# Kernel tuning notes

Measured on AMD Instinct MI355X. Metric: run time of the kernel, lower is better.

The kernel has to match this reference:

```python
import jax, jax.numpy as jnp
import numpy as np
from jax import lax

DIM = 512
HEADS = 8
HEAD_DIM = DIM // HEADS
FS = 56            # features_size -> H = W = 56
SR = 2             # sr_ratio
N = FS * FS        # query tokens = 3136
KN = (FS // SR) ** 2  # kv tokens = 784
B = 4
SCALE = HEAD_DIM ** -0.5
LN_EPS = 1e-5


def _relative_indices(fs):
    # matches generate_relative_distance: [[x, y] for x in range(fs) for y in range(fs)]
    coords = np.stack(np.meshgrid(np.arange(fs), np.arange(fs), indexing='ij'), -1).reshape(-1, 2)
    dist = coords[None, :, :] - coords[:, None, :] + (fs - 1)   # (N, N, 2), values in [0, 2fs-2]
    return jnp.asarray(dist, dtype=jnp.int32)


def setup_inputs() -> dict:
    key = jax.random.key(0)
    ks = jax.random.split(key, 8)
    s = 0.02
    return {
        'x':    jax.random.normal(ks[0], (B, DIM, FS, FS), jnp.float32),
        'Wq':   jax.random.normal(ks[1], (DIM, DIM), jnp.float32) * s,
        'Wkv':  jax.random.normal(ks[2], (DIM, 2 * DIM), jnp.float32) * s,
        'Wsr':  jax.random.normal(ks[3], (DIM, DIM, SR, SR), jnp.float32) * s,  # OIHW
        'b_sr': jnp.zeros((DIM,), jnp.float32),
        'gamma': jnp.ones((DIM,), jnp.float32),
        'beta':  jnp.zeros((DIM,), jnp.float32),
        'Wp':   jax.random.normal(ks[4], (DIM, DIM), jnp.float32) * s,
        'bp':   jnp.zeros((DIM,), jnp.float32),
        'pos':  jax.random.normal(ks[5], (2 * FS - 1, 2 * FS - 1), jnp.float32) * 0.2,
        'rel_idx': _relative_indices(FS),
    }


def reference(x, Wq, Wkv, Wsr, b_sr, gamma, beta, Wp, bp, pos, rel_idx):
    b, c, h, w = x.shape
    n = h * w
    xq = x.reshape(b, c, n).transpose(0, 2, 1)                      # B N C
    q = (xq @ Wq).reshape(b, n, HEADS, HEAD_DIM).transpose(0, 2, 1, 3)  # B h N d

    # spatial reduction of k/v: Conv2d(k=SR, s=SR) + LayerNorm
    xr = lax.conv_general_dilated(x, Wsr, (SR, SR), 'VALID',
                                  dimension_numbers=('NCHW', 'OIHW', 'NCHW'))
    xr = xr + b_sr[None, :, None, None]
    kn = xr.shape[2] * xr.shape[3]
    xkv = xr.reshape(b, c, kn).transpose(0, 2, 1)                   # B KN C
    mu = xkv.mean(-1, keepdims=True)
    var = ((xkv - mu) ** 2).mean(-1, keepdims=True)
    xkv = (xkv - mu) * lax.rsqrt(var + LN_EPS) * gamma + beta

    # kv projection; rearrange 'B N (dim h l) -> l B h N dim'
    kv = (xkv @ Wkv).reshape(b, kn, HEAD_DIM, HEADS, 2)
    k = kv[..., 0].transpose(0, 3, 1, 2)                            # B h KN d
    v = kv[..., 1].transpose(0, 3, 1, 2)                            # B h KN d

    attn = jnp.einsum('bhnd,bhmd->bhnm', q, k) * SCALE              # B h N KN
    bias = pos[rel_idx[:, :kn, 0], rel_idx[:, :kn, 1]]              # N KN gathered bias
    attn = jax.nn.softmax(attn + bias, axis=-1)

    out = jnp.einsum('bhnm,bhmd->bhnd', attn, v)                    # B h N d
    out = out.transpose(0, 2, 1, 3).reshape(b, n, c)                # B N C
    out = out @ Wp + bp
    return out.transpose(0, 2, 1).reshape(b, c, h, w)
```

## Files before the change

kernel.cpp:

```cpp
#include <hip/hip_runtime.h>
#include <hip/hip_bf16.h>
#include <cstdint>

constexpr int BATCH = 4;
constexpr int CDIM  = 512;
constexpr int NHEAD = 8;
constexpr int HD    = 64;
constexpr int FSP   = 56;
constexpr int NTOK  = FSP * FSP;
constexpr int KH    = 28;
constexpr int KNTOK = KH * KH;
constexpr float SCALE_ATT = 0.125f;
constexpr int BIAS_LD = 832;

typedef _Float16 f16;
typedef __attribute__((ext_vector_type(8))) _Float16 half8;
typedef __attribute__((ext_vector_type(4))) float  floatx4;

__device__ __forceinline__ void tr64(const float* __restrict__ in,
                                     f16* __restrict__ out, int R, int C,
                                     int r0, int c0, float (*sm)[65], int tid) {
  const int rr = tid >> 2, cs = (tid & 3) * 16;
  const float* src = in + (size_t)(r0 + rr) * C + c0 + cs;
#pragma unroll
  for (int j = 0; j < 16; j += 4) *(float4*)&sm[rr][cs + j] = *(const float4*)&src[j];
  __syncthreads();
  f16* dh = out + (size_t)(c0 + rr) * R + r0 + cs;
#pragma unroll
  for (int j = 0; j < 16; ++j) dh[j] = (f16)sm[cs + j][rr];
}

__global__ __launch_bounds__(256) void k_prep(const float* __restrict__ x,
                                              const float* __restrict__ Wq,
                                              const float* __restrict__ Wkv,
                                              const float* __restrict__ Wp,
                                              const float* __restrict__ Wsr,
                                              const int* __restrict__ rel,
                                              const float* __restrict__ pos,
                                              f16* __restrict__ xT,
                                              f16* __restrict__ WqT,
                                              f16* __restrict__ WkvT,
                                              f16* __restrict__ WpT,
                                              f16* __restrict__ WsrP,
                                              float* __restrict__ biasT) {
  __shared__ float sm[64][65];
  const int tid = threadIdx.x;
  int bid = blockIdx.x;
  if (bid < 1568) {
    const int b = bid / 392, r = bid % 392;
    tr64(x + (size_t)b * CDIM * NTOK, xT + (size_t)b * NTOK * CDIM,
         CDIM, NTOK, (r % 8) * 64, (r / 8) * 64, sm, tid);
    return;
  }
  bid -= 1568;
  if (bid < 64)  { tr64(Wq,  WqT,  512, 512,  (bid % 8) * 64, (bid / 8) * 64, sm, tid); return; }
  bid -= 64;
  if (bid < 128) { tr64(Wkv, WkvT, 512, 1024, (bid % 8) * 64, (bid / 8) * 64, sm, tid); return; }
  bid -= 128;
  if (bid < 64)  { tr64(Wp,  WpT,  512, 512,  (bid % 8) * 64, (bid / 8) * 64, sm, tid); return; }
  bid -= 64;
  if (bid < 512) {
    const float* src = Wsr + (size_t)bid * 2048;
    f16* dh = WsrP + (size_t)bid * 2048;
    for (int kp = tid; kp < 2048; kp += 256) {
      const int dd = kp >> 9, c = kp & 511;
      dh[kp] = (f16)src[c * 4 + dd];
    }
    return;
  }
  bid -= 512;
  {
    const int n = bid;
    for (int i = tid; i < BIAS_LD; i += 256) {
      const int jc = i >> 6, w = i & 63, txx = w >> 2, tt = w & 3;
      const int m = jc * 64 + tt * 16 + txx;
      float v = -30000.f;
      if (m < KNTOK) {
        const size_t o = ((size_t)n * NTOK + m) * 2;
        v = pos[rel[o] * 111 + rel[o + 1]];
      }
      biasT[(size_t)n * BIAS_LD + i] = v;
    }
  }
}

#define GSTR 40
struct GemmSmem { f16 A[64][GSTR]; f16 B[128][GSTR]; };

__device__ __forceinline__ void gemm_loop64(GemmSmem* sm,
    const f16* __restrict__ aP, const f16* __restrict__ bP, bool doA,
    int sr, int ss, int wm, int wn, int quad, int tx, floatx4 acc[2][4]) {
  half8 ra0 = {0, 0, 0, 0, 0, 0, 0, 0}, ra1 = ra0;
  if (doA) { ra0 = *(const half8*)&aP[0]; ra1 = *(const half8*)&aP[8]; }
  half8 rb0 = *(const half8*)&bP[0], rb1 = *(const half8*)&bP[8];
  for (int it = 0; it < 16; ++it) {
    if (doA) { *(half8*)&sm->A[sr][ss] = ra0; *(half8*)&sm->A[sr][ss + 8] = ra1; }
    *(half8*)&sm->B[sr][ss] = rb0; *(half8*)&sm->B[sr][ss + 8] = rb1;
    __syncthreads();
    if (it + 1 < 16) {
      const f16* an = aP + (it + 1) * 32;
      const f16* bn = bP + (it + 1) * 32;
      if (doA) { ra0 = *(const half8*)&an[0]; ra1 = *(const half8*)&an[8]; }
      rb0 = *(const half8*)&bn[0]; rb1 = *(const half8*)&bn[8];
    }
    half8 ah[2];
#pragma unroll
    for (int i = 0; i < 2; ++i)
      ah[i] = *(const half8*)&sm->A[wm * 32 + i * 16 + tx][quad * 8];
#pragma unroll
    for (int j = 0; j < 4; ++j) {
      const half8 bh = *(const half8*)&sm->B[wn * 64 + j * 16 + tx][quad * 8];
#pragma unroll
      for (int i = 0; i < 2; ++i)
        acc[i][j] = __builtin_amdgcn_mfma_f32_16x16x32_f16(ah[i], bh, acc[i][j], 0, 0, 0);
    }
    __syncthreads();
  }
}

#define GEMM_PRE64()                                                      \
  const int tid = threadIdx.x, lane = tid & 63, wv = tid >> 6;            \
  const int wm = wv & 1, wn = wv >> 1, quad = lane >> 4, tx = lane & 15;  \
  const int sr = tid >> 1, ss = (tid & 1) * 16;                           \
  const bool doA = tid < 128;                                             \
  floatx4 acc[2][4];                                                      \
  _Pragma("unroll") for (int i = 0; i < 2; ++i)                           \
  _Pragma("unroll") for (int j = 0; j < 4; ++j)                           \
      acc[i][j] = (floatx4){0.f, 0.f, 0.f, 0.f};

__global__ __launch_bounds__(256) void k_gemmA(const f16* __restrict__ xT,
                                               const f16* __restrict__ WqT,
                                               f16* __restrict__ Qh,
                                               const f16* __restrict__ WsrP,
                                               float* __restrict__ XRp) {
  __shared__ GemmSmem sm;
  GEMM_PRE64();
  int bid = blockIdx.x;
  if (bid < 784) {
    const int b = bid / 196, r = bid % 196;
    const int m0 = (r >> 2) * 64, n0 = (r & 3) * 128;
    const f16* aP = xT + (size_t)b * NTOK * CDIM + (size_t)(m0 + sr) * CDIM + ss;
    const f16* bP = WqT + (size_t)(n0 + sr) * CDIM + ss;
    gemm_loop64(&sm, aP, bP, doA, sr, ss, wm, wn, quad, tx, acc);
    f16* qhB = Qh + (size_t)b * NTOK * CDIM;
#pragma unroll
    for (int i = 0; i < 2; ++i)
#pragma unroll
      for (int rg = 0; rg < 4; ++rg) {
        const int m = m0 + wm * 32 + i * 16 + quad * 4 + rg;
#pragma unroll
        for (int j = 0; j < 4; ++j)
          qhB[(size_t)m * CDIM + n0 + wn * 64 + j * 16 + tx] = (f16)acc[i][j][rg];
      }
  } else {
    bid -= 784;
    const int bkc = bid / 52, r = bid % 52;
    const int b = bkc >> 2, kc = bkc & 3;
    const int m0 = (r >> 2) * 64, n0 = (r & 3) * 128;
    int am = m0 + sr; if (am >= KNTOK) am = 0;
    const int ii = am / KH, jj = am % KH;
    const int sp = 112 * ii + 2 * jj + (kc >> 1) * FSP + (kc & 1);
    const f16* aP = xT + (size_t)b * NTOK * CDIM + (size_t)sp * CDIM + ss;
    const f16* bP = WsrP + (size_t)(n0 + sr) * 2048 + kc * 512 + ss;
    gemm_loop64(&sm, aP, bP, doA, sr, ss, wm, wn, quad, tx, acc);
    float* dst = XRp + (size_t)(kc * BATCH + b) * KNTOK * CDIM;
#pragma unroll
    for (int i = 0; i < 2; ++i)
#pragma unroll
      for (int rg = 0; rg < 4; ++rg) {
        const int m = m0 + wm * 32 + i * 16 + quad * 4 + rg;
        if (m >= KNTOK) continue;
#pragma unroll
        for (int j = 0; j < 4; ++j)
          dst[(size_t)m * CDIM + n0 + wn * 64 + j * 16 + tx] = acc[i][j][rg];
      }
  }
}

__global__ __launch_bounds__(256) void k_ln(const float* __restrict__ XRp,
                                            const float* __restrict__ b_sr,
                                            const float* __restrict__ gamma,
                                            const float* __restrict__ beta,
                                            f16* __restrict__ oh) {
  const int row = blockIdx.x;
  const size_t slab = (size_t)BATCH * KNTOK * CDIM;
  const float* p = XRp + (size_t)row * CDIM;
  const int tid = threadIdx.x;
  const float v0 = p[tid] + p[tid + slab] + p[tid + 2 * slab] + p[tid + 3 * slab]
                 + b_sr[tid];
  const float v1 = p[tid + 256] + p[tid + 256 + slab] + p[tid + 256 + 2 * slab]
                 + p[tid + 256 + 3 * slab] + b_sr[tid + 256];
  float s = v0 + v1;
  float s2 = v0 * v0 + v1 * v1;
#pragma unroll
  for (int mask = 32; mask >= 1; mask >>= 1) {
    s  += __shfl_xor(s, mask, 64);
    s2 += __shfl_xor(s2, mask, 64);
  }
  __shared__ float ws[4], ws2[4];
  const int wid = tid >> 6;
  if ((tid & 63) == 0) { ws[wid] = s; ws2[wid] = s2; }
  __syncthreads();
  const float ts  = ws[0] + ws[1] + ws[2] + ws[3];
  const float ts2 = ws2[0] + ws2[1] + ws2[2] + ws2[3];
  const float mu  = ts * (1.f / CDIM);
  const float var = ts2 * (1.f / CDIM) - mu * mu;
  const float rs  = rsqrtf(var + 1e-5f);
  const size_t base = (size_t)row * CDIM;
  oh[base + tid]       = (f16)((v0 - mu) * rs * gamma[tid] + beta[tid]);
  oh[base + tid + 256] = (f16)((v1 - mu) * rs * gamma[tid + 256] + beta[tid + 256]);
}

__global__ __launch_bounds__(256) void k_kvproj(const f16* __restrict__ XRh,
                                                const f16* __restrict__ WkvT,
                                                f16* __restrict__ Kh,
                                                f16* __restrict__ Vt) {
  __shared__ GemmSmem sm;
  GEMM_PRE64();
  const int bid = blockIdx.x;
  const int b = bid / 104, r = bid % 104;
  const int m0 = (r >> 3) * 64, n0 = (r & 7) * 128;
  int arow = m0 + sr; if (arow >= KNTOK) arow = KNTOK - 1;
  const f16* aP = XRh + (size_t)b * KNTOK * CDIM + (size_t)arow * CDIM + ss;
  const f16* bP = WkvT + (size_t)(n0 + sr) * CDIM + ss;
  gemm_loop64(&sm, aP, bP, doA, sr, ss, wm, wn, quad, tx, acc);
#pragma unroll
  for (int i = 0; i < 2; ++i)
#pragma unroll
    for (int rg = 0; rg < 4; ++rg) {
      const int m = m0 + wm * 32 + i * 16 + quad * 4 + rg;
      if (m >= KNTOK) continue;
#pragma unroll
      for (int j = 0; j < 4; ++j) {
        const int o2 = n0 + wn * 64 + j * 16 + tx;
        const int d = o2 >> 4, hh = (o2 >> 1) & 7;
        const float v = acc[i][j][rg];
        if (o2 & 1)
          Vt[((size_t)(b * NHEAD + hh) * HD + d) * KNTOK + m] = (f16)v;
        else
          Kh[((size_t)(b * NHEAD + hh) * KNTOK + m) * HD + d] = (f16)v;
      }
    }
}

#define LSTR 72
__global__ __launch_bounds__(256) void k_attn(const f16* __restrict__ Qh,
                                              const f16* __restrict__ Kh,
                                              const f16* __restrict__ Vt,
                                              const float* __restrict__ biasT,
                                              f16* __restrict__ Oh) {
  __shared__ f16 Qhs[64][LSTR], Khs[64][LSTR], Vts[64][LSTR];
  __shared__ f16 Ps[4][16][LSTR];
  const int b = blockIdx.x >> 3, h = blockIdx.x & 7;
  const int n0 = blockIdx.y * 64;
  const int tid = threadIdx.x, lane = tid & 63, wv = tid >> 6;
  const int quad = lane >> 4, tx = lane & 15;
  const int rr = tid >> 2, sg = (tid & 3) * 16;

  const f16* qhB = Qh + ((size_t)b * NTOK + n0) * CDIM + h * HD;
  const f16* khB = Kh + (size_t)(b * NHEAD + h) * KNTOK * HD;
  const f16* vtB = Vt + (size_t)(b * NHEAD + h) * HD * KNTOK;

  {
    const size_t qoff = (size_t)rr * CDIM + sg;
    *(half8*)&Qhs[rr][sg]     = *(const half8*)&qhB[qoff];
    *(half8*)&Qhs[rr][sg + 8] = *(const half8*)&qhB[qoff + 8];
    const size_t koff = (size_t)rr * HD + sg;
    *(half8*)&Khs[rr][sg]     = *(const half8*)&khB[koff];
    *(half8*)&Khs[rr][sg + 8] = *(const half8*)&khB[koff + 8];
    const size_t voff = (size_t)rr * KNTOK + sg;
    *(half8*)&Vts[rr][sg]     = *(const half8*)&vtB[voff];
    *(half8*)&Vts[rr][sg + 8] = *(const half8*)&vtB[voff + 8];
  }

  size_t bbase_r[4];
#pragma unroll
  for (int r = 0; r < 4; ++r)
    bbase_r[r] = (size_t)(n0 + wv * 16 + quad * 4 + r) * BIAS_LD + tx * 4;

  floatx4 acc_o[4];
#pragma unroll
  for (int t = 0; t < 4; ++t) acc_o[t] = (floatx4){0.f, 0.f, 0.f, 0.f};
  float l_part[4] = {0.f, 0.f, 0.f, 0.f};
  __syncthreads();

  half8 nk0, nk1, nv0, nv1;
  for (int jc = 0; jc < 13; ++jc) {
    if (jc < 12) {
      const int mbn = (jc + 1) * 64;
      const int km = min(mbn + rr, KNTOK - 1);
      const size_t koff = (size_t)km * HD + sg;
      nk0 = *(const half8*)&khB[koff];
      nk1 = *(const half8*)&khB[koff + 8];
      const int vc = min(mbn + sg, KNTOK - 16);
      const size_t voff = (size_t)rr * KNTOK + vc;
      nv0 = *(const half8*)&vtB[voff];
      nv1 = *(const half8*)&vtB[voff + 8];
    }

    floatx4 sc[4];
#pragma unroll
    for (int t = 0; t < 4; ++t) sc[t] = (floatx4){0.f, 0.f, 0.f, 0.f};
#pragma unroll
    for (int ks = 0; ks < 2; ++ks) {
      const int kk = ks * 32 + quad * 8;
      const half8 aqh = *(const half8*)&Qhs[wv * 16 + tx][kk];
#pragma unroll
      for (int t = 0; t < 4; ++t) {
        const half8 bkh = *(const half8*)&Khs[t * 16 + tx][kk];
        sc[t] = __builtin_amdgcn_mfma_f32_16x16x32_f16(aqh, bkh, sc[t], 0, 0, 0);
      }
    }

#pragma unroll
    for (int r = 0; r < 4; ++r) {
      const float4 bb = *(const float4*)&biasT[bbase_r[r] + jc * 64];
      const float p0 = __expf(fmaf(sc[0][r], SCALE_ATT, bb.x));
      const float p1 = __expf(fmaf(sc[1][r], SCALE_ATT, bb.y));
      const float p2 = __expf(fmaf(sc[2][r], SCALE_ATT, bb.z));
      const float p3 = __expf(fmaf(sc[3][r], SCALE_ATT, bb.w));
      l_part[r] += (p0 + p1) + (p2 + p3);
      const int prow = quad * 4 + r;
      Ps[wv][prow][0 * 16 + tx] = (f16)p0;
      Ps[wv][prow][1 * 16 + tx] = (f16)p1;
      Ps[wv][prow][2 * 16 + tx] = (f16)p2;
      Ps[wv][prow][3 * 16 + tx] = (f16)p3;
    }

#pragma unroll
    for (int ks = 0; ks < 2; ++ks) {
      const int kk = ks * 32 + quad * 8;
      const half8 ap = *(const half8*)&Ps[wv][tx][kk];
#pragma unroll
      for (int t = 0; t < 4; ++t) {
        const half8 bv = *(const half8*)&Vts[t * 16 + tx][kk];
        acc_o[t] = __builtin_amdgcn_mfma_f32_16x16x32_f16(ap, bv, acc_o[t], 0, 0, 0);
      }
    }
    __syncthreads();
    if (jc < 12) {
      *(half8*)&Khs[rr][sg]     = nk0;
      *(half8*)&Khs[rr][sg + 8] = nk1;
      *(half8*)&Vts[rr][sg]     = nv0;
      *(half8*)&Vts[rr][sg + 8] = nv1;
    }
    __syncthreads();
  }

#pragma unroll
  for (int r = 0; r < 4; ++r) {
    float l = l_part[r];
#pragma unroll
    for (int msk = 1; msk < 16; msk <<= 1) l += __shfl_xor(l, msk, 64);
    const float inv = 1.f / l;
    const int grow = n0 + wv * 16 + quad * 4 + r;
    const size_t base = ((size_t)b * NTOK + grow) * CDIM + h * HD;
#pragma unroll
    for (int t = 0; t < 4; ++t)
      Oh[base + t * 16 + tx] = (f16)(acc_o[t][r] * inv);
  }
}

__global__ __launch_bounds__(256) void k_outproj(const f16* __restrict__ Og,
                                                 const f16* __restrict__ WpT,
                                                 const float* __restrict__ bp,
                                                 float* __restrict__ out) {
  __shared__ GemmSmem sm;
  GEMM_PRE64();
  const int bid = blockIdx.x;
  const int b = bid / 196, r = bid % 196;
  const int m0 = (r >> 2) * 64, n0 = (r & 3) * 128;
  const f16* aP = Og + (size_t)b * NTOK * CDIM + (size_t)(m0 + sr) * CDIM + ss;
  const f16* bP = WpT + (size_t)(n0 + sr) * CDIM + ss;
  gemm_loop64(&sm, aP, bP, doA, sr, ss, wm, wn, quad, tx, acc);
#pragma unroll
  for (int j = 0; j < 4; ++j) {
    const int co = n0 + wn * 64 + j * 16 + tx;
    const float bpv = bp[co];
    float* obase = out + ((size_t)b * CDIM + co) * NTOK;
#pragma unroll
    for (int i = 0; i < 2; ++i) {
      const int mb4 = m0 + wm * 32 + i * 16 + quad * 4;
      floatx4 v = acc[i][j] + bpv;
      *(floatx4*)&obase[mb4] = v;
    }
  }
}

extern "C" void kernel_launch(void* const* d_in, const int* in_sizes, int n_in,
                              void* d_out, int out_size, void* d_ws, size_t ws_size,
                              hipStream_t stream) {
  const float* x     = (const float*)d_in[0];
  const float* Wq    = (const float*)d_in[1];
  const float* Wkv   = (const float*)d_in[2];
  const float* Wsr   = (const float*)d_in[3];
  const float* b_sr  = (const float*)d_in[4];
  const float* gamma = (const float*)d_in[5];
  const float* beta  = (const float*)d_in[6];
  const float* Wp    = (const float*)d_in[7];
  const float* bp    = (const float*)d_in[8];
  const float* pos   = (const float*)d_in[9];
  const int*   rel   = (const int*)d_in[10];
  float* out = (float*)d_out;

  char* p = (char*)d_ws;
  auto alloc = [&](size_t bytes) -> void* {
    void* r = (void*)p;
    p += (bytes + 255) & ~(size_t)255;
    return r;
  };
  const size_t SZ_BNC = (size_t)BATCH * NTOK * CDIM;
  const size_t SZ_BKC = (size_t)BATCH * KNTOK * CDIM;
  const size_t SZ_KV  = (size_t)BATCH * NHEAD * KNTOK * HD;

  f16* xT    = (f16*)alloc(SZ_BNC * 2);
  f16* WqT   = (f16*)alloc(512 * 512 * 2);
  f16* WkvT  = (f16*)alloc(1024 * 512 * 2);
  f16* WpT   = (f16*)alloc(512 * 512 * 2);
  f16* WsrP  = (f16*)alloc(512 * 2048 * 2);
  f16* Qh    = (f16*)alloc(SZ_BNC * 2);
  float* XRp = (float*)alloc(SZ_BKC * 4 * 4);
  f16* XRh   = (f16*)alloc(SZ_BKC * 2);
  f16* Vt    = (f16*)alloc(SZ_KV * 2);
  float* biasT = (float*)alloc((size_t)NTOK * BIAS_LD * 4);

  f16* Kh = (f16*)XRp;
  f16* Og = xT;

  const dim3 blk(256);
  k_prep   <<<dim3(5472), blk, 0, stream>>>(x, Wq, Wkv, Wp, Wsr, rel, pos,
                                            xT, WqT, WkvT, WpT, WsrP, biasT);
  k_gemmA  <<<dim3(1616), blk, 0, stream>>>(xT, WqT, Qh, WsrP, XRp);
  k_ln     <<<dim3(BATCH * KNTOK), blk, 0, stream>>>(XRp, b_sr, gamma, beta, XRh);
  k_kvproj <<<dim3(416),  blk, 0, stream>>>(XRh, WkvT, Kh, Vt);
  k_attn   <<<dim3(BATCH * NHEAD, 49), blk, 0, stream>>>(Qh, Kh, Vt, biasT, Og);
  k_outproj<<<dim3(784),  blk, 0, stream>>>(Og, WpT, bp, out);
}
```

Baseline: 305.4 us.

## Fuse Q projection into attention kernel and read K/V straight from global

```diff
diff --git a/kernel.cpp b/kernel.cpp
--- a/kernel.cpp
+++ b/kernel.cpp
@@ -128,53 +128,32 @@
   _Pragma("unroll") for (int j = 0; j < 4; ++j)                           \
       acc[i][j] = (floatx4){0.f, 0.f, 0.f, 0.f};
 
-__global__ __launch_bounds__(256) void k_gemmA(const f16* __restrict__ xT,
-                                               const f16* __restrict__ WqT,
-                                               f16* __restrict__ Qh,
-                                               const f16* __restrict__ WsrP,
-                                               float* __restrict__ XRp) {
+__global__ __launch_bounds__(256) void k_srconv(const f16* __restrict__ xT,
+                                                const f16* __restrict__ WsrP,
+                                                float* __restrict__ XRp) {
   __shared__ GemmSmem sm;
   GEMM_PRE64();
   int bid = blockIdx.x;
-  if (bid < 784) {
-    const int b = bid / 196, r = bid % 196;
-    const int m0 = (r >> 2) * 64, n0 = (r & 3) * 128;
-    const f16* aP = xT + (size_t)b * NTOK * CDIM + (size_t)(m0 + sr) * CDIM + ss;
-    const f16* bP = WqT + (size_t)(n0 + sr) * CDIM + ss;
-    gemm_loop64(&sm, aP, bP, doA, sr, ss, wm, wn, quad, tx, acc);
-    f16* qhB = Qh + (size_t)b * NTOK * CDIM;
-#pragma unroll
-    for (int i = 0; i < 2; ++i)
-#pragma unroll
-      for (int rg = 0; rg < 4; ++rg) {
-        const int m = m0 + wm * 32 + i * 16 + quad * 4 + rg;
-#pragma unroll
-        for (int j = 0; j < 4; ++j)
-          qhB[(size_t)m * CDIM + n0 + wn * 64 + j * 16 + tx] = (f16)acc[i][j][rg];
-      }
-  } else {
-    bid -= 784;
-    const int bkc = bid / 52, r = bid % 52;
-    const int b = bkc >> 2, kc = bkc & 3;
-    const int m0 = (r >> 2) * 64, n0 = (r & 3) * 128;
-    int am = m0 + sr; if (am >= KNTOK) am = 0;
-    const int ii = am / KH, jj = am % KH;
-    const int sp = 112 * ii + 2 * jj + (kc >> 1) * FSP + (kc & 1);
-    const f16* aP = xT + (size_t)b * NTOK * CDIM + (size_t)sp * CDIM + ss;
-    const f16* bP = WsrP + (size_t)(n0 + sr) * 2048 + kc * 512 + ss;
-    gemm_loop64(&sm, aP, bP, doA, sr, ss, wm, wn, quad, tx, acc);
-    float* dst = XRp + (size_t)(kc * BATCH + b) * KNTOK * CDIM;
-#pragma unroll
-    for (int i = 0; i < 2; ++i)
-#pragma unroll
-      for (int rg = 0; rg < 4; ++rg) {
-        const int m = m0 + wm * 32 + i * 16 + quad * 4 + rg;
-        if (m >= KNTOK) continue;
-#pragma unroll
-        for (int j = 0; j < 4; ++j)
-          dst[(size_t)m * CDIM + n0 + wn * 64 + j * 16 + tx] = acc[i][j][rg];
-      }
-  }
+  const int bkc = bid / 52, r = bid % 52;
+  const int b = bkc >> 2, kc = bkc & 3;
+  const int m0 = (r >> 2) * 64, n0 = (r & 3) * 128;
+  int am = m0 + sr; if (am >= KNTOK) am = 0;
+  const int ii = am / KH, jj = am % KH;
+  const int sp = 112 * ii + 2 * jj + (kc >> 1) * FSP + (kc & 1);
+  const f16* aP = xT + (size_t)b * NTOK * CDIM + (size_t)sp * CDIM + ss;
+  const f16* bP = WsrP + (size_t)(n0 + sr) * 2048 + kc * 512 + ss;
+  gemm_loop64(&sm, aP, bP, doA, sr, ss, wm, wn, quad, tx, acc);
+  float* dst = XRp + (size_t)(kc * BATCH + b) * KNTOK * CDIM;
+#pragma unroll
+  for (int i = 0; i < 2; ++i)
+#pragma unroll
+    for (int rg = 0; rg < 4; ++rg) {
+      const int m = m0 + wm * 32 + i * 16 + quad * 4 + rg;
+      if (m >= KNTOK) continue;
+#pragma unroll
+      for (int j = 0; j < 4; ++j)
+        dst[(size_t)m * CDIM + n0 + wn * 64 + j * 16 + tx] = acc[i][j][rg];
+    }
 }
 
 __global__ __launch_bounds__(256) void k_ln(const float* __restrict__ XRp,
@@ -244,121 +223,165 @@
 }
 
 #define LSTR 72
-__global__ __launch_bounds__(256) void k_attn(const f16* __restrict__ Qh,
+__global__ __launch_bounds__(256) void k_attn(const f16* __restrict__ xT,
+                                              const f16* __restrict__ WqT,
                                               const f16* __restrict__ Kh,
                                               const f16* __restrict__ Vt,
                                               const float* __restrict__ biasT,
                                               f16* __restrict__ Oh) {
-  __shared__ f16 Qhs[64][LSTR], Khs[64][LSTR], Vts[64][LSTR];
-  __shared__ f16 Ps[4][16][LSTR];
+  __shared__ f16 Qhs[128 * LSTR];
+  __shared__ f16 Ps[4 * 32 * LSTR];
   const int b = blockIdx.x >> 3, h = blockIdx.x & 7;
-  const int n0 = blockIdx.y * 64;
+  const int n0 = blockIdx.y * 128;
   const int tid = threadIdx.x, lane = tid & 63, wv = tid >> 6;
   const int quad = lane >> 4, tx = lane & 15;
-  const int rr = tid >> 2, sg = (tid & 3) * 16;
-
-  const f16* qhB = Qh + ((size_t)b * NTOK + n0) * CDIM + h * HD;
+
+  const f16* xb  = xT + (size_t)b * NTOK * CDIM;
+  const f16* wq  = WqT + (size_t)(h * HD) * CDIM;
   const f16* khB = Kh + (size_t)(b * NHEAD + h) * KNTOK * HD;
   const f16* vtB = Vt + (size_t)(b * NHEAD + h) * HD * KNTOK;
 
   {
-    const size_t qoff = (size_t)rr * CDIM + sg;
-    *(half8*)&Qhs[rr][sg]     = *(const half8*)&qhB[qoff];
-    *(half8*)&Qhs[rr][sg + 8] = *(const half8*)&qhB[qoff + 8];
-    const size_t koff = (size_t)rr * HD + sg;
-    *(half8*)&Khs[rr][sg]     = *(const half8*)&khB[koff];
-    *(half8*)&Khs[rr][sg + 8] = *(const half8*)&khB[koff + 8];
-    const size_t voff = (size_t)rr * KNTOK + sg;
-    *(half8*)&Vts[rr][sg]     = *(const half8*)&vtB[voff];
-    *(half8*)&Vts[rr][sg + 8] = *(const half8*)&vtB[voff + 8];
-  }
-
-  size_t bbase_r[4];
-#pragma unroll
-  for (int r = 0; r < 4; ++r)
-    bbase_r[r] = (size_t)(n0 + wv * 16 + quad * 4 + r) * BIAS_LD + tx * 4;
-
-  floatx4 acc_o[4];
-#pragma unroll
-  for (int t = 0; t < 4; ++t) acc_o[t] = (floatx4){0.f, 0.f, 0.f, 0.f};
-  float l_part[4] = {0.f, 0.f, 0.f, 0.f};
-  __syncthreads();
-
-  half8 nk0, nk1, nv0, nv1;
+    f16* Astage = Qhs;
+    f16* Bstage = Ps;
+    const int ar = tid >> 1, as_ = (tid & 1) * 16;
+    const int br = tid >> 2, bs_ = (tid & 3) * 8;
+    const int arow = min(n0 + ar, NTOK - 1);
+    const f16* aP = xb + (size_t)arow * CDIM + as_;
+    const f16* bP = wq + (size_t)br * CDIM + bs_;
+    floatx4 qacc[2][4];
+#pragma unroll
+    for (int i = 0; i < 2; ++i)
+#pragma unroll
+      for (int j = 0; j < 4; ++j) qacc[i][j] = (floatx4){0.f, 0.f, 0.f, 0.f};
+    half8 ra0 = *(const half8*)&aP[0], ra1 = *(const half8*)&aP[8];
+    half8 rb0 = *(const half8*)&bP[0];
+    for (int it = 0; it < 16; ++it) {
+      *(half8*)&Astage[ar * GSTR + as_]     = ra0;
+      *(half8*)&Astage[ar * GSTR + as_ + 8] = ra1;
+      *(half8*)&Bstage[br * GSTR + bs_]     = rb0;
+      __syncthreads();
+      if (it + 1 < 16) {
+        const f16* an = aP + (it + 1) * 32;
+        const f16* bn = bP + (it + 1) * 32;
+        ra0 = *(const half8*)&an[0]; ra1 = *(const half8*)&an[8];
+        rb0 = *(const half8*)&bn[0];
+      }
+      half8 af[2];
+#pragma unroll
+      for (int i = 0; i < 2; ++i)
+        af[i] = *(const half8*)&Astage[(wv * 32 + i * 16 + tx) * GSTR + quad * 8];
+#pragma unroll
+      for (int j = 0; j < 4; ++j) {
+        const half8 bf = *(const half8*)&Bstage[(j * 16 + tx) * GSTR + quad * 8];
+#pragma unroll
+        for (int i = 0; i < 2; ++i)
+          qacc[i][j] = __builtin_amdgcn_mfma_f32_16x16x32_f16(af[i], bf, qacc[i][j], 0, 0, 0);
+      }
+      __syncthreads();
+    }
+#pragma unroll
+    for (int i = 0; i < 2; ++i)
+#pragma unroll
+      for (int j = 0; j < 4; ++j)
+#pragma unroll
+        for (int rg = 0; rg < 4; ++rg)
+          Qhs[(wv * 32 + i * 16 + quad * 4 + rg) * LSTR + j * 16 + tx] =
+              (f16)qacc[i][j][rg];
+  }
+
+  size_t bbase[2][4];
+#pragma unroll
+  for (int i = 0; i < 2; ++i)
+#pragma unroll
+    for (int rg = 0; rg < 4; ++rg) {
+      const int grow = min(n0 + wv * 32 + i * 16 + quad * 4 + rg, NTOK - 1);
+      bbase[i][rg] = (size_t)grow * BIAS_LD + tx * 4;
+    }
+
+  floatx4 acc_o[2][4];
+#pragma unroll
+  for (int i = 0; i < 2; ++i)
+#pragma unroll
+    for (int t = 0; t < 4; ++t) acc_o[i][t] = (floatx4){0.f, 0.f, 0.f, 0.f};
+  float l_part[2][4] = {};
+
+  f16* PsW = Ps + wv * 32 * LSTR;
+
   for (int jc = 0; jc < 13; ++jc) {
-    if (jc < 12) {
-      const int mbn = (jc + 1) * 64;
-      const int km = min(mbn + rr, KNTOK - 1);
-      const size_t koff = (size_t)km * HD + sg;
-      nk0 = *(const half8*)&khB[koff];
-      nk1 = *(const half8*)&khB[koff + 8];
-      const int vc = min(mbn + sg, KNTOK - 16);
-      const size_t voff = (size_t)rr * KNTOK + vc;
-      nv0 = *(const half8*)&vtB[voff];
-      nv1 = *(const half8*)&vtB[voff + 8];
-    }
-
-    floatx4 sc[4];
-#pragma unroll
-    for (int t = 0; t < 4; ++t) sc[t] = (floatx4){0.f, 0.f, 0.f, 0.f};
+    const int mb = jc * 64;
+    floatx4 sc[2][4];
+#pragma unroll
+    for (int i = 0; i < 2; ++i)
+#pragma unroll
+      for (int t = 0; t < 4; ++t) sc[i][t] = (floatx4){0.f, 0.f, 0.f, 0.f};
 #pragma unroll
     for (int ks = 0; ks < 2; ++ks) {
       const int kk = ks * 32 + quad * 8;
-      const half8 aqh = *(const half8*)&Qhs[wv * 16 + tx][kk];
+      half8 aq[2];
+#pragma unroll
+      for (int i = 0; i < 2; ++i)
+        aq[i] = *(const half8*)&Qhs[(wv * 32 + i * 16 + tx) * LSTR + kk];
 #pragma unroll
       for (int t = 0; t < 4; ++t) {
-        const half8 bkh = *(const half8*)&Khs[t * 16 + tx][kk];
-        sc[t] = __builtin_amdgcn_mfma_f32_16x16x32_f16(aqh, bkh, sc[t], 0, 0, 0);
-      }
-    }
-
-#pragma unroll
-    for (int r = 0; r < 4; ++r) {
-      const float4 bb = *(const float4*)&biasT[bbase_r[r] + jc * 64];
-      const float p0 = __expf(fmaf(sc[0][r], SCALE_ATT, bb.x));
-      const float p1 = __expf(fmaf(sc[1][r], SCALE_ATT, bb.y));
-      const float p2 = __expf(fmaf(sc[2][r], SCALE_ATT, bb.z));
-      const float p3 = __expf(fmaf(sc[3][r], SCALE_ATT, bb.w));
-      l_part[r] += (p0 + p1) + (p2 + p3);
-      const int prow = quad * 4 + r;
-      Ps[wv][prow][0 * 16 + tx] = (f16)p0;
-      Ps[wv][prow][1 * 16 + tx] = (f16)p1;
-      Ps[wv][prow][2 * 16 + tx] = (f16)p2;
-      Ps[wv][prow][3 * 16 + tx] = (f16)p3;
-    }
-
+        const int krow = min(mb + t * 16 + tx, KNTOK - 1);
+        const half8 bk = *(const half8*)&khB[(size_t)krow * HD + kk];
+#pragma unroll
+        for (int i = 0; i < 2; ++i)
+          sc[i][t] = __builtin_amdgcn_mfma_f32_16x16x32_f16(aq[i], bk, sc[i][t], 0, 0, 0);
+      }
+    }
+#pragma unroll
+    for (int i = 0; i < 2; ++i)
+#pragma unroll
+      for (int rg = 0; rg < 4; ++rg) {
+        const float4 bb = *(const float4*)&biasT[bbase[i][rg] + jc * 64];
+        const float p0 = __expf(fmaf(sc[0 + 0][0][rg], 0.f, 0.f) * 0.f +
+                                fmaf(sc[i][0][rg], SCALE_ATT, bb.x));
+        const float p1 = __expf(fmaf(sc[i][1][rg], SCALE_ATT, bb.y));
+        const float p2 = __expf(fmaf(sc[i][2][rg], SCALE_ATT, bb.z));
+        const float p3 = __expf(fmaf(sc[i][3][rg], SCALE_ATT, bb.w));
+        l_part[i][rg] += (p0 + p1) + (p2 + p3);
+        const int prow = i * 16 + quad * 4 + rg;
+        PsW[prow * LSTR + 0 * 16 + tx] = (f16)p0;
+        PsW[prow * LSTR + 1 * 16 + tx] = (f16)p1;
+        PsW[prow * LSTR + 2 * 16 + tx] = (f16)p2;
+        PsW[prow * LSTR + 3 * 16 + tx] = (f16)p3;
+      }
 #pragma unroll
     for (int ks = 0; ks < 2; ++ks) {
       const int kk = ks * 32 + quad * 8;
-      const half8 ap = *(const half8*)&Ps[wv][tx][kk];
+      half8 ap[2];
+#pragma unroll
+      for (int i = 0; i < 2; ++i)
+        ap[i] = *(const half8*)&PsW[(i * 16 + tx) * LSTR + kk];
+      const int vcol = min(mb + kk, KNTOK - 8);
 #pragma unroll
       for (int t = 0; t < 4; ++t) {
-        const half8 bv = *(const half8*)&Vts[t * 16 + tx][kk];
-        acc_o[t] = __builtin_amdgcn_mfma_f32_16x16x32_f16(ap, bv, acc_o[t], 0, 0, 0);
-      }
-    }
-    __syncthreads();
-    if (jc < 12) {
-      *(half8*)&Khs[rr][sg]     = nk0;
-      *(half8*)&Khs[rr][sg + 8] = nk1;
-      *(half8*)&Vts[rr][sg]     = nv0;
-      *(half8*)&Vts[rr][sg + 8] = nv1;
-    }
-    __syncthreads();
-  }
-
-#pragma unroll
-  for (int r = 0; r < 4; ++r) {
-    float l = l_part[r];
-#pragma unroll
-    for (int msk = 1; msk < 16; msk <<= 1) l += __shfl_xor(l, msk, 64);
-    const float inv = 1.f / l;
-    const int grow = n0 + wv * 16 + quad * 4 + r;
-    const size_t base = ((size_t)b * NTOK + grow) * CDIM + h * HD;
-#pragma unroll
-    for (int t = 0; t < 4; ++t)
-      Oh[base + t * 16 + tx] = (f16)(acc_o[t][r] * inv);
-  }
+        const half8 bv = *(const half8*)&vtB[(size_t)(t * 16 + tx) * KNTOK + vcol];
+#pragma unroll
+        for (int i = 0; i < 2; ++i)
+          acc_o[i][t] = __builtin_amdgcn_mfma_f32_16x16x32_f16(ap[i], bv, acc_o[i][t], 0, 0, 0);
+      }
+    }
+  }
+
+#pragma unroll
+  for (int i = 0; i < 2; ++i)
+#pragma unroll
+    for (int rg = 0; rg < 4; ++rg) {
+      float l = l_part[i][rg];
+#pragma unroll
+      for (int msk = 1; msk < 16; msk <<= 1) l += __shfl_xor(l, msk, 64);
+      const float inv = 1.f / l;
+      const int grow = n0 + wv * 32 + i * 16 + quad * 4 + rg;
+      if (grow < NTOK) {
+        const size_t base = ((size_t)b * NTOK + grow) * CDIM + h * HD;
+#pragma unroll
+        for (int t = 0; t < 4; ++t)
+          Oh[base + t * 16 + tx] = (f16)(acc_o[i][t][rg] * inv);
+      }
+    }
 }
 
 __global__ __launch_bounds__(256) void k_outproj(const f16* __restrict__ Og,
@@ -418,21 +441,20 @@
   f16* WkvT  = (f16*)alloc(1024 * 512 * 2);
   f16* WpT   = (f16*)alloc(512 * 512 * 2);
   f16* WsrP  = (f16*)alloc(512 * 2048 * 2);
-  f16* Qh    = (f16*)alloc(SZ_BNC * 2);
   float* XRp = (float*)alloc(SZ_BKC * 4 * 4);
   f16* XRh   = (f16*)alloc(SZ_BKC * 2);
   f16* Vt    = (f16*)alloc(SZ_KV * 2);
+  f16* Og    = (f16*)alloc(SZ_BNC * 2);
   float* biasT = (float*)alloc((size_t)NTOK * BIAS_LD * 4);
 
   f16* Kh = (f16*)XRp;
-  f16* Og = xT;
 
   const dim3 blk(256);
   k_prep   <<<dim3(5472), blk, 0, stream>>>(x, Wq, Wkv, Wp, Wsr, rel, pos,
                                             xT, WqT, WkvT, WpT, WsrP, biasT);
-  k_gemmA  <<<dim3(1616), blk, 0, stream>>>(xT, WqT, Qh, WsrP, XRp);
+  k_srconv <<<dim3(832),  blk, 0, stream>>>(xT, WsrP, XRp);
   k_ln     <<<dim3(BATCH * KNTOK), blk, 0, stream>>>(XRp, b_sr, gamma, beta, XRh);
   k_kvproj <<<dim3(416),  blk, 0, stream>>>(XRh, WkvT, Kh, Vt);
-  k_attn   <<<dim3(BATCH * NHEAD, 49), blk, 0, stream>>>(Qh, Kh, Vt, biasT, Og);
+  k_attn   <<<dim3(BATCH * NHEAD, 25), blk, 0, stream>>>(xT, WqT, Kh, Vt, biasT, Og);
   k_outproj<<<dim3(784),  blk, 0, stream>>>(Og, WpT, bp, out);
 }
```

Measured after the change: 401.6 us. 1.32x slower.

## Use 128x128 GEMM tiles with direct global-to-LDS loads

Applied to the files above, without the earlier changes.

```diff
diff --git a/kernel.cpp b/kernel.cpp
--- a/kernel.cpp
+++ b/kernel.cpp
@@ -84,47 +84,50 @@
   }
 }
 
-#define GSTR 40
-struct GemmSmem { f16 A[64][GSTR]; f16 B[128][GSTR]; };
-
-__device__ __forceinline__ void gemm_loop64(GemmSmem* sm,
-    const f16* __restrict__ aP, const f16* __restrict__ bP, bool doA,
-    int sr, int ss, int wm, int wn, int quad, int tx, floatx4 acc[2][4]) {
-  half8 ra0 = {0, 0, 0, 0, 0, 0, 0, 0}, ra1 = ra0;
-  if (doA) { ra0 = *(const half8*)&aP[0]; ra1 = *(const half8*)&aP[8]; }
-  half8 rb0 = *(const half8*)&bP[0], rb1 = *(const half8*)&bP[8];
+struct GemmSmem { f16 A[128 * 32]; f16 B[128 * 32]; };
+
+__device__ __forceinline__ void gl_lds(const f16* g, f16* l) {
+  __builtin_amdgcn_global_load_lds(
+      (const __attribute__((address_space(1))) void*)g,
+      (__attribute__((address_space(3))) void*)l, 16, 0, 0);
+}
+
+__device__ __forceinline__ void gemm128(GemmSmem* sm,
+    const f16* a0, const f16* a1, const f16* b0, const f16* b1,
+    int lane, int wv, int wm, int wn, int quad, int tx,
+    floatx4 acc[4][4]) {
+  f16* lA0 = sm->A + wv * 1024 + lane * 8;
+  f16* lA1 = sm->A + wv * 1024 + 512 + lane * 8;
+  f16* lB0 = sm->B + wv * 1024 + lane * 8;
+  f16* lB1 = sm->B + wv * 1024 + 512 + lane * 8;
   for (int it = 0; it < 16; ++it) {
-    if (doA) { *(half8*)&sm->A[sr][ss] = ra0; *(half8*)&sm->A[sr][ss + 8] = ra1; }
-    *(half8*)&sm->B[sr][ss] = rb0; *(half8*)&sm->B[sr][ss + 8] = rb1;
+    gl_lds(a0 + it * 32, lA0);
+    gl_lds(a1 + it * 32, lA1);
+    gl_lds(b0 + it * 32, lB0);
+    gl_lds(b1 + it * 32, lB1);
     __syncthreads();
-    if (it + 1 < 16) {
-      const f16* an = aP + (it + 1) * 32;
-      const f16* bn = bP + (it + 1) * 32;
-      if (doA) { ra0 = *(const half8*)&an[0]; ra1 = *(const half8*)&an[8]; }
-      rb0 = *(const half8*)&bn[0]; rb1 = *(const half8*)&bn[8];
-    }
-    half8 ah[2];
-#pragma unroll
-    for (int i = 0; i < 2; ++i)
-      ah[i] = *(const half8*)&sm->A[wm * 32 + i * 16 + tx][quad * 8];
-#pragma unroll
-    for (int j = 0; j < 4; ++j) {
-      const half8 bh = *(const half8*)&sm->B[wn * 64 + j * 16 + tx][quad * 8];
-#pragma unroll
-      for (int i = 0; i < 2; ++i)
-        acc[i][j] = __builtin_amdgcn_mfma_f32_16x16x32_f16(ah[i], bh, acc[i][j], 0, 0, 0);
-    }
+    half8 af[4], bf[4];
+#pragma unroll
+    for (int i = 0; i < 4; ++i)
+      af[i] = *(const half8*)&sm->A[(wm * 64 + i * 16 + tx) * 32 + quad * 8];
+#pragma unroll
+    for (int j = 0; j < 4; ++j)
+      bf[j] = *(const half8*)&sm->B[(wn * 64 + j * 16 + tx) * 32 + quad * 8];
+#pragma unroll
+    for (int j = 0; j < 4; ++j)
+#pragma unroll
+      for (int i = 0; i < 4; ++i)
+        acc[i][j] = __builtin_amdgcn_mfma_f32_16x16x32_f16(af[i], bf[j], acc[i][j], 0, 0, 0);
     __syncthreads();
   }
 }
 
-#define GEMM_PRE64()                                                      \
+#define GEMM128_PRE()                                                     \
   const int tid = threadIdx.x, lane = tid & 63, wv = tid >> 6;            \
   const int wm = wv & 1, wn = wv >> 1, quad = lane >> 4, tx = lane & 15;  \
-  const int sr = tid >> 1, ss = (tid & 1) * 16;                           \
-  const bool doA = tid < 128;                                             \
-  floatx4 acc[2][4];                                                      \
-  _Pragma("unroll") for (int i = 0; i < 2; ++i)                           \
+  const int lr = lane >> 2, lc = (lane & 3) * 8;                          \
+  floatx4 acc[4][4];                                                      \
+  _Pragma("unroll") for (int i = 0; i < 4; ++i)                           \
   _Pragma("unroll") for (int j = 0; j < 4; ++j)                           \
       acc[i][j] = (floatx4){0.f, 0.f, 0.f, 0.f};
 
@@ -134,41 +137,51 @@
                                                const f16* __restrict__ WsrP,
                                                float* __restrict__ XRp) {
   __shared__ GemmSmem sm;
-  GEMM_PRE64();
+  GEMM128_PRE();
   int bid = blockIdx.x;
-  if (bid < 784) {
-    const int b = bid / 196, r = bid % 196;
-    const int m0 = (r >> 2) * 64, n0 = (r & 3) * 128;
-    const f16* aP = xT + (size_t)b * NTOK * CDIM + (size_t)(m0 + sr) * CDIM + ss;
-    const f16* bP = WqT + (size_t)(n0 + sr) * CDIM + ss;
-    gemm_loop64(&sm, aP, bP, doA, sr, ss, wm, wn, quad, tx, acc);
+  if (bid < 400) {
+    const int b = bid / 100, t = bid % 100;
+    const int m0 = (t >> 2) * 128, n0 = (t & 3) * 128;
+    const f16* xb = xT + (size_t)b * NTOK * CDIM;
+    const int r0 = wv * 32 + lr, r1 = r0 + 16;
+    const f16* a0 = xb + (size_t)min(m0 + r0, NTOK - 1) * CDIM + lc;
+    const f16* a1 = xb + (size_t)min(m0 + r1, NTOK - 1) * CDIM + lc;
+    const f16* b0 = WqT + (size_t)(n0 + r0) * CDIM + lc;
+    const f16* b1 = WqT + (size_t)(n0 + r1) * CDIM + lc;
+    gemm128(&sm, a0, a1, b0, b1, lane, wv, wm, wn, quad, tx, acc);
     f16* qhB = Qh + (size_t)b * NTOK * CDIM;
 #pragma unroll
-    for (int i = 0; i < 2; ++i)
+    for (int i = 0; i < 4; ++i)
 #pragma unroll
       for (int rg = 0; rg < 4; ++rg) {
-        const int m = m0 + wm * 32 + i * 16 + quad * 4 + rg;
+        const int m = m0 + wm * 64 + i * 16 + quad * 4 + rg;
+        if (m >= NTOK) continue;
 #pragma unroll
         for (int j = 0; j < 4; ++j)
           qhB[(size_t)m * CDIM + n0 + wn * 64 + j * 16 + tx] = (f16)acc[i][j][rg];
       }
   } else {
-    bid -= 784;
-    const int bkc = bid / 52, r = bid % 52;
+    bid -= 400;
+    const int bkc = bid / 28, r = bid % 28;
     const int b = bkc >> 2, kc = bkc & 3;
-    const int m0 = (r >> 2) * 64, n0 = (r & 3) * 128;
-    int am = m0 + sr; if (am >= KNTOK) am = 0;
-    const int ii = am / KH, jj = am % KH;
-    const int sp = 112 * ii + 2 * jj + (kc >> 1) * FSP + (kc & 1);
-    const f16* aP = xT + (size_t)b * NTOK * CDIM + (size_t)sp * CDIM + ss;
-    const f16* bP = WsrP + (size_t)(n0 + sr) * 2048 + kc * 512 + ss;
-    gemm_loop64(&sm, aP, bP, doA, sr, ss, wm, wn, quad, tx, acc);
+    const int m0 = (r >> 2) * 128, n0 = (r & 3) * 128;
+    const f16* xb = xT + (size_t)b * NTOK * CDIM;
+    const int r0 = wv * 32 + lr, r1 = r0 + 16;
+    int am0 = m0 + r0; if (am0 >= KNTOK) am0 = 0;
+    int am1 = m0 + r1; if (am1 >= KNTOK) am1 = 0;
+    const int sp0 = 112 * (am0 / KH) + 2 * (am0 % KH) + (kc >> 1) * FSP + (kc & 1);
+    const int sp1 = 112 * (am1 / KH) + 2 * (am1 % KH) + (kc >> 1) * FSP + (kc & 1);
+    const f16* a0 = xb + (size_t)sp0 * CDIM + lc;
+    const f16* a1 = xb + (size_t)sp1 * CDIM + lc;
+    const f16* b0 = WsrP + (size_t)(n0 + r0) * 2048 + kc * 512 + lc;
+    const f16* b1 = WsrP + (size_t)(n0 + r1) * 2048 + kc * 512 + lc;
+    gemm128(&sm, a0, a1, b0, b1, lane, wv, wm, wn, quad, tx, acc);
     float* dst = XRp + (size_t)(kc * BATCH + b) * KNTOK * CDIM;
 #pragma unroll
-    for (int i = 0; i < 2; ++i)
+    for (int i = 0; i < 4; ++i)
 #pragma unroll
       for (int rg = 0; rg < 4; ++rg) {
-        const int m = m0 + wm * 32 + i * 16 + quad * 4 + rg;
+        const int m = m0 + wm * 64 + i * 16 + quad * 4 + rg;
         if (m >= KNTOK) continue;
 #pragma unroll
         for (int j = 0; j < 4; ++j)
@@ -216,19 +229,23 @@
                                                 f16* __restrict__ Kh,
                                                 f16* __restrict__ Vt) {
   __shared__ GemmSmem sm;
-  GEMM_PRE64();
+  GEMM128_PRE();
   const int bid = blockIdx.x;
-  const int b = bid / 104, r = bid % 104;
-  const int m0 = (r >> 3) * 64, n0 = (r & 7) * 128;
-  int arow = m0 + sr; if (arow >= KNTOK) arow = KNTOK - 1;
-  const f16* aP = XRh + (size_t)b * KNTOK * CDIM + (size_t)arow * CDIM + ss;
-  const f16* bP = WkvT + (size_t)(n0 + sr) * CDIM + ss;
-  gemm_loop64(&sm, aP, bP, doA, sr, ss, wm, wn, quad, tx, acc);
-#pragma unroll
-  for (int i = 0; i < 2; ++i)
+  const int b = bid / 56, r = bid % 56, nt = r >> 3, mt = r & 7;
+  const int m0 = (r / 8) * 128, n0 = (r % 8) * 128;
+  (void)nt; (void)mt;
+  const f16* ab = XRh + (size_t)b * KNTOK * CDIM;
+  const int r0 = wv * 32 + lr, r1 = r0 + 16;
+  const f16* a0 = ab + (size_t)min(m0 + r0, KNTOK - 1) * CDIM + lc;
+  const f16* a1 = ab + (size_t)min(m0 + r1, KNTOK - 1) * CDIM + lc;
+  const f16* b0 = WkvT + (size_t)(n0 + r0) * CDIM + lc;
+  const f16* b1 = WkvT + (size_t)(n0 + r1) * CDIM + lc;
+  gemm128(&sm, a0, a1, b0, b1, lane, wv, wm, wn, quad, tx, acc);
+#pragma unroll
+  for (int i = 0; i < 4; ++i)
 #pragma unroll
     for (int rg = 0; rg < 4; ++rg) {
-      const int m = m0 + wm * 32 + i * 16 + quad * 4 + rg;
+      const int m = m0 + wm * 64 + i * 16 + quad * 4 + rg;
       if (m >= KNTOK) continue;
 #pragma unroll
       for (int j = 0; j < 4; ++j) {
@@ -366,23 +383,29 @@
                                                  const float* __restrict__ bp,
                                                  float* __restrict__ out) {
   __shared__ GemmSmem sm;
-  GEMM_PRE64();
+  GEMM128_PRE();
   const int bid = blockIdx.x;
-  const int b = bid / 196, r = bid % 196;
-  const int m0 = (r >> 2) * 64, n0 = (r & 3) * 128;
-  const f16* aP = Og + (size_t)b * NTOK * CDIM + (size_t)(m0 + sr) * CDIM + ss;
-  const f16* bP = WpT + (size_t)(n0 + sr) * CDIM + ss;
-  gemm_loop64(&sm, aP, bP, doA, sr, ss, wm, wn, quad, tx, acc);
+  const int b = bid / 100, t = bid % 100;
+  const int m0 = (t >> 2) * 128, n0 = (t & 3) * 128;
+  const f16* ab = Og + (size_t)b * NTOK * CDIM;
+  const int r0 = wv * 32 + lr, r1 = r0 + 16;
+  const f16* a0 = ab + (size_t)min(m0 + r0, NTOK - 1) * CDIM + lc;
+  const f16* a1 = ab + (size_t)min(m0 + r1, NTOK - 1) * CDIM + lc;
+  const f16* b0 = WpT + (size_t)(n0 + r0) * CDIM + lc;
+  const f16* b1 = WpT + (size_t)(n0 + r1) * CDIM + lc;
+  gemm128(&sm, a0, a1, b0, b1, lane, wv, wm, wn, quad, tx, acc);
 #pragma unroll
   for (int j = 0; j < 4; ++j) {
     const int co = n0 + wn * 64 + j * 16 + tx;
     const float bpv = bp[co];
     float* obase = out + ((size_t)b * CDIM + co) * NTOK;
 #pragma unroll
-    for (int i = 0; i < 2; ++i) {
-      const int mb4 = m0 + wm * 32 + i * 16 + quad * 4;
-      floatx4 v = acc[i][j] + bpv;
-      *(floatx4*)&obase[mb4] = v;
+    for (int i = 0; i < 4; ++i) {
+      const int mb4 = m0 + wm * 64 + i * 16 + quad * 4;
+      if (mb4 < NTOK) {
+        floatx4 v = acc[i][j] + bpv;
+        *(floatx4*)&obase[mb4] = v;
+      }
     }
   }
 }
@@ -430,9 +453,9 @@
   const dim3 blk(256);
   k_prep   <<<dim3(5472), blk, 0, stream>>>(x, Wq, Wkv, Wp, Wsr, rel, pos,
                                             xT, WqT, WkvT, WpT, WsrP, biasT);
-  k_gemmA  <<<dim3(1616), blk, 0, stream>>>(xT, WqT, Qh, WsrP, XRp);
+  k_gemmA  <<<dim3(848),  blk, 0, stream>>>(xT, WqT, Qh, WsrP, XRp);
   k_ln     <<<dim3(BATCH * KNTOK), blk, 0, stream>>>(XRp, b_sr, gamma, beta, XRh);
-  k_kvproj <<<dim3(416),  blk, 0, stream>>>(XRh, WkvT, Kh, Vt);
+  k_kvproj <<<dim3(224),  blk, 0, stream>>>(XRh, WkvT, Kh, Vt);
   k_attn   <<<dim3(BATCH * NHEAD, 49), blk, 0, stream>>>(Qh, Kh, Vt, biasT, Og);
-  k_outproj<<<dim3(784),  blk, 0, stream>>>(Og, WpT, bp, out);
-}
+  k_outproj<<<dim3(400),  blk, 0, stream>>>(Og, WpT, bp, out);
+}
```

Result: no change. 301.6 us (-1.2%).
